# Kernel tuning notes

Measured on AMD Instinct MI355X. Metric: run time of the kernel, lower is better.

Reference implementation:

```python
import jax, jax.numpy as jnp
import numpy as np

# Static conv / spline hyperparameters (match init_kwargs)
KH = KW = 3
SH = SW = 1          # stride
DH = DW = 1          # dilation
GRID_SIZE = 5
SPLINE_ORDER = 3
N_CONVS = 8


def _extract_patches(x):
    """im2col unfold. x: (B,C,H,W) -> (B,C,Ho,Wo,KH*KW), valid padding."""
    B, C, H, W = x.shape
    Ho = (H - (KH - 1) * DH - 1) // SH + 1
    Wo = (W - (KW - 1) * DW - 1) // SW + 1
    cols = []
    for i in range(KH):
        for j in range(KW):
            cols.append(x[:, :,
                          i * DH: i * DH + (Ho - 1) * SH + 1: SH,
                          j * DW: j * DW + (Wo - 1) * SW + 1: SW])
    return jnp.stack(cols, axis=-1), Ho, Wo


def _b_splines(xf, grid):
    """Cox-de Boor recursion. xf: (P,K), grid: (K, G+2*so+1) -> (P,K,G+so)."""
    x = xf[:, :, None]
    bases = ((x >= grid[:, :-1]) & (x < grid[:, 1:])).astype(xf.dtype)
    for k in range(1, SPLINE_ORDER + 1):
        bases = ((x - grid[:, :-(k + 1)]) / (grid[:, k:-1] - grid[:, :-(k + 1)])
                 * bases[:, :, :-1]
                 + (grid[:, k + 1:] - x) / (grid[:, k + 1:] - grid[:, 1:-k])
                 * bases[:, :, 1:])
    return bases


def setup_inputs() -> dict:
    key = jax.random.key(0)
    k0, k1, k2, k3 = jax.random.split(key, 4)
    B, C, H, W = 8, 32, 64, 64
    K = KH * KW                       # in_features of KANLinear = 9
    coeff = GRID_SIZE + SPLINE_ORDER  # spline coefficients per input = 8
    # activations inside grid_range [-1, 1]
    x = jax.random.uniform(k0, (B, C, H, W), jnp.float32, -1.0, 1.0)
    # grid buffer: arange(-so, gs+so+1)*h + grid_range[0], tiled per input feature
    h = (1.0 - (-1.0)) / GRID_SIZE
    g = jnp.arange(-SPLINE_ORDER, GRID_SIZE + SPLINE_ORDER + 1,
                   dtype=jnp.float32) * h - 1.0
    grid = jnp.tile(g[None, :], (K, 1))  # (K, 12)
    base_weight = jax.random.normal(k1, (N_CONVS, K), jnp.float32) / np.sqrt(K)
    spline_weight = jax.random.normal(k2, (N_CONVS, K, coeff), jnp.float32) * 0.1
    spline_scaler = jax.random.normal(k3, (N_CONVS, K), jnp.float32) / np.sqrt(K) + 1.0
    return {"x": x, "grid": grid, "base_weight": base_weight,
            "spline_weight": spline_weight, "spline_scaler": spline_scaler}


def reference(x, grid, base_weight, spline_weight, spline_scaler):
    B, C, H, W = x.shape
    patches, Ho, Wo = _extract_patches(x)          # (B,C,Ho,Wo,K)
    K = KH * KW
    xf = patches.reshape(-1, K)                    # (P, K), P = B*C*Ho*Wo
    # KANLinear: base path (SiLU + linear) + spline path (B-spline basis + linear)
    base_out = jnp.einsum('pk,vk->pv', jax.nn.silu(xf), base_weight)
    bases = _b_splines(xf, grid)                   # (P, K, coeff)
    scaled_sw = spline_weight * spline_scaler[:, :, None]
    spline_out = jnp.einsum('pkc,vkc->pv', bases, scaled_sw)
    out = (base_out + spline_out).reshape(B, C, Ho, Wo, N_CONVS)
    # channel-major then conv ordering: out[:, kern + channel*n_convs]
    return out.transpose(0, 1, 4, 2, 3).reshape(B, C * N_CONVS, Ho, Wo)
```

## Files before the change

kernel.cpp:

```cpp
#include <hip/hip_runtime.h>

typedef _Float16 f16;
typedef _Float16 f16x8 __attribute__((ext_vector_type(8)));
typedef float    f32x4 __attribute__((ext_vector_type(4)));

#define HO 62
#define WO 62

__global__ __launch_bounds__(256, 4) void kan_conv_mfma2(
    const float* __restrict__ x,
    const float* __restrict__ grid,
    const float* __restrict__ bw,
    const float* __restrict__ sw,
    const float* __restrict__ sc,
    float* __restrict__ out)
{
    __shared__ __align__(16) f16 feat[10368];

    const int tid  = threadIdx.x;
    const int lane = tid & 63;
    const int w    = tid >> 6;

    const int bx    = blockIdx.x;
    const int plane = bx >> 3;
    const int chunk = bx & 7;
    const int r0    = chunk * 8;

    const int nn = lane & 15;
    const int kb = lane >> 4;
    f16x8 bfrag[3][2];
    #pragma unroll
    for (int ki = 0; ki < 3; ++ki) {
        #pragma unroll
        for (int kjp = 0; kjp < 2; ++kjp) {
            f16x8 bf;
            #pragma unroll
            for (int e = 0; e < 8; ++e) {
                const int k    = kb * 8 + e;
                const int kj   = kjp * 2 + (k >> 4);
                const int slot = k & 15;
                float wv = 0.0f;
                if (nn < 8 && kj < 3 && slot < 9) {
                    const int kk = ki * 3 + kj;
                    wv = (slot == 0) ? bw[nn * 9 + kk]
                                     : sw[(nn * 9 + kk) * 8 + (slot - 1)] * sc[nn * 9 + kk];
                }
                bf[e] = (f16)wv;
            }
            bfrag[ki][kjp] = bf;
        }
    }

    const float g0    = grid[0];
    const float inv_h = 1.0f / (grid[1] - grid[0]);
    const float* xp   = x + (size_t)plane * 4096;

    for (int idx = tid; idx < 640; idx += 256) {
        const int row = idx >> 6;
        const int col = idx & 63;
        int gy = r0 + row; gy = (gy < 64) ? gy : 63;
        const float xv = xp[gy * 64 + col];

        const float s = xv / (1.0f + __expf(-xv));
        const float u = (xv - g0) * inv_h;
        int j = (int)floorf(u);
        j = (j < 3) ? 3 : ((j > 7) ? 7 : j);
        const float t   = u - (float)j;
        const float omt = 1.0f - t;
        const float t2  = t * t;
        const float t3  = t2 * t;
        const float c6  = 1.0f / 6.0f;
        float bv[4];
        bv[0] = omt * omt * omt * c6;
        bv[1] = (3.0f * t3 - 6.0f * t2 + 4.0f) * c6;
        bv[2] = (-3.0f * t3 + 3.0f * t2 + 3.0f * t + 1.0f) * c6;
        bv[3] = t3 * c6;

        const int base0 = row * 1024 + col * 8;
        f16x8 z0 = {(f16)s, (f16)0.f, (f16)0.f, (f16)0.f,
                    (f16)0.f, (f16)0.f, (f16)0.f, (f16)0.f};
        f16x8 z1 = {(f16)0.f, (f16)0.f, (f16)0.f, (f16)0.f,
                    (f16)0.f, (f16)0.f, (f16)0.f, (f16)0.f};
        *(f16x8*)&feat[base0]       = z0;
        *(f16x8*)&feat[base0 + 512] = z1;
        #pragma unroll
        for (int m = 0; m < 4; ++m) {
            const int slot = j - 2 + m;
            feat[row * 1024 + (slot >> 3) * 512 + col * 8 + (slot & 7)] = (f16)bv[m];
        }
    }
    if (tid < 16) {
        f16x8 z = {(f16)0.f, (f16)0.f, (f16)0.f, (f16)0.f,
                   (f16)0.f, (f16)0.f, (f16)0.f, (f16)0.f};
        *(f16x8*)&feat[10240 + tid * 8] = z;
    }
    __syncthreads();

    const int mI    = lane & 15;
    const int khalf = kb & 1;
    const int cAdd  = kb >> 1;
    const int c0    = w * 16;
    const int aBase = khalf * 512 + (c0 + mI + cAdd) * 8;

    f16x8 af[3][2];
    #pragma unroll
    for (int kjp = 0; kjp < 2; ++kjp) {
        af[0][kjp] = *(const f16x8*)&feat[aBase + kjp * 16 + 0 * 1024];
        af[1][kjp] = *(const f16x8*)&feat[aBase + kjp * 16 + 1 * 1024];
    }

    #pragma unroll
    for (int i = 0; i < 8; ++i) {
        #pragma unroll
        for (int kjp = 0; kjp < 2; ++kjp)
            af[(i + 2) % 3][kjp] = *(const f16x8*)&feat[aBase + kjp * 16 + (i + 2) * 1024];

        f32x4 acc = {0.f, 0.f, 0.f, 0.f};
        #pragma unroll
        for (int ki = 0; ki < 3; ++ki) {
            #pragma unroll
            for (int kjp = 0; kjp < 2; ++kjp)
                acc = __builtin_amdgcn_mfma_f32_16x16x32_f16(
                          af[(i + ki) % 3][kjp], bfrag[ki][kjp], acc, 0, 0, 0);
        }

        const int ho = r0 + i;
        if (nn < 8 && ho < HO) {
            const int cb = c0 + kb * 4;
            float* po = out + ((size_t)(plane * 8 + nn) * (HO * WO)) + ho * WO + cb;
            if (cb + 3 < WO) {
                float2 lo = {acc[0], acc[1]};
                float2 hi = {acc[2], acc[3]};
                *(float2*)po       = lo;
                *(float2*)(po + 2) = hi;
            } else {
                #pragma unroll
                for (int q = 0; q < 4; ++q)
                    if (cb + q < WO) po[q] = acc[q];
            }
        }
    }
}

extern "C" void kernel_launch(void* const* d_in, const int* in_sizes, int n_in,
                              void* d_out, int out_size, void* d_ws, size_t ws_size,
                              hipStream_t stream) {
    const float* x    = (const float*)d_in[0];
    const float* grid = (const float*)d_in[1];
    const float* bw   = (const float*)d_in[2];
    const float* sw   = (const float*)d_in[3];
    const float* sc   = (const float*)d_in[4];
    float* out = (float*)d_out;

    kan_conv_mfma2<<<2048, 256, 0, stream>>>(x, grid, bw, sw, sc, out);
}
```

Measured before the change: 97.16 us.

## Give each wavefront a private feature tile to drop the block barrier

Each wavefront now computes SiLU and B-spline features for its own 10x18 halo tile into a private LDS slice. This removes the __syncthreads between feature construction and the MFMA stage, and lays features out as contiguous 16-element records per pixel. The cost is recomputing halo columns, about 180 features per wave instead of 160, and the launch bound rises to 5 blocks per CU. It relies on wavefront-level execution ordering instead of an explicit barrier for LDS visibility within the wave.

```diff
diff --git a/kernel.cpp b/kernel.cpp
--- a/kernel.cpp
+++ b/kernel.cpp
@@ -7,7 +7,7 @@
 #define HO 62
 #define WO 62
 
-__global__ __launch_bounds__(256, 4) void kan_conv_mfma2(
+__global__ __launch_bounds__(256, 5) void kan_conv_nobar(
     const float* __restrict__ x,
     const float* __restrict__ grid,
     const float* __restrict__ bw,
@@ -15,16 +15,18 @@
     const float* __restrict__ sc,
     float* __restrict__ out)
 {
-    __shared__ __align__(16) f16 feat[10368];
+    __shared__ __align__(16) f16 feat[4 * 2880];
 
     const int tid  = threadIdx.x;
     const int lane = tid & 63;
     const int w    = tid >> 6;
+    f16* wfeat = &feat[w * 2880];
 
     const int bx    = blockIdx.x;
     const int plane = bx >> 3;
     const int chunk = bx & 7;
     const int r0    = chunk * 8;
+    const int c0    = w * 16;
 
     const int nn = lane & 15;
     const int kb = lane >> 4;
@@ -51,69 +53,74 @@
         }
     }
 
+    const float* xp = x + (size_t)plane * 4096;
+    float xv3[3];
+    int   p3[3];
+    #pragma unroll
+    for (int it = 0; it < 3; ++it) {
+        int p = it * 64 + lane;
+        p3[it] = p;
+        int row = p / 18;
+        int col = p - row * 18;
+        int gy = r0 + row; gy = (gy < 64) ? gy : 63;
+        int gx = c0 + col; gx = (gx < 64) ? gx : 63;
+        xv3[it] = xp[gy * 64 + gx];
+    }
+
     const float g0    = grid[0];
     const float inv_h = 1.0f / (grid[1] - grid[0]);
-    const float* xp   = x + (size_t)plane * 4096;
 
-    for (int idx = tid; idx < 640; idx += 256) {
-        const int row = idx >> 6;
-        const int col = idx & 63;
-        int gy = r0 + row; gy = (gy < 64) ? gy : 63;
-        const float xv = xp[gy * 64 + col];
+    #pragma unroll
+    for (int it = 0; it < 3; ++it) {
+        const int p = p3[it];
+        if (p < 180) {
+            const float xv = xv3[it];
+            const float s = xv / (1.0f + __expf(-xv));
+            const float u = (xv - g0) * inv_h;
+            int j = (int)floorf(u);
+            j = (j < 3) ? 3 : ((j > 7) ? 7 : j);
+            const float t   = u - (float)j;
+            const float omt = 1.0f - t;
+            const float t2  = t * t;
+            const float t3  = t2 * t;
+            const float c6  = 1.0f / 6.0f;
+            float bv0 = omt * omt * omt * c6;
+            float bv1 = (3.0f * t3 - 6.0f * t2 + 4.0f) * c6;
+            float bv2 = (-3.0f * t3 + 3.0f * t2 + 3.0f * t + 1.0f) * c6;
+            float bv3 = t3 * c6;
 
-        const float s = xv / (1.0f + __expf(-xv));
-        const float u = (xv - g0) * inv_h;
-        int j = (int)floorf(u);
-        j = (j < 3) ? 3 : ((j > 7) ? 7 : j);
-        const float t   = u - (float)j;
-        const float omt = 1.0f - t;
-        const float t2  = t * t;
-        const float t3  = t2 * t;
-        const float c6  = 1.0f / 6.0f;
-        float bv[4];
-        bv[0] = omt * omt * omt * c6;
-        bv[1] = (3.0f * t3 - 6.0f * t2 + 4.0f) * c6;
-        bv[2] = (-3.0f * t3 + 3.0f * t2 + 3.0f * t + 1.0f) * c6;
-        bv[3] = t3 * c6;
-
-        const int base0 = row * 1024 + col * 8;
-        f16x8 z0 = {(f16)s, (f16)0.f, (f16)0.f, (f16)0.f,
-                    (f16)0.f, (f16)0.f, (f16)0.f, (f16)0.f};
-        f16x8 z1 = {(f16)0.f, (f16)0.f, (f16)0.f, (f16)0.f,
-                    (f16)0.f, (f16)0.f, (f16)0.f, (f16)0.f};
-        *(f16x8*)&feat[base0]       = z0;
-        *(f16x8*)&feat[base0 + 512] = z1;
-        #pragma unroll
-        for (int m = 0; m < 4; ++m) {
-            const int slot = j - 2 + m;
-            feat[row * 1024 + (slot >> 3) * 512 + col * 8 + (slot & 7)] = (f16)bv[m];
+            f16* fp = &wfeat[p * 16];
+            f16x8 z0 = {(f16)s, (f16)0.f, (f16)0.f, (f16)0.f,
+                        (f16)0.f, (f16)0.f, (f16)0.f, (f16)0.f};
+            f16x8 z1 = {(f16)0.f, (f16)0.f, (f16)0.f, (f16)0.f,
+                        (f16)0.f, (f16)0.f, (f16)0.f, (f16)0.f};
+            *(f16x8*)fp       = z0;
+            *(f16x8*)(fp + 8) = z1;
+            fp[j - 2] = (f16)bv0;
+            fp[j - 1] = (f16)bv1;
+            fp[j]     = (f16)bv2;
+            fp[j + 1] = (f16)bv3;
         }
     }
-    if (tid < 16) {
-        f16x8 z = {(f16)0.f, (f16)0.f, (f16)0.f, (f16)0.f,
-                   (f16)0.f, (f16)0.f, (f16)0.f, (f16)0.f};
-        *(f16x8*)&feat[10240 + tid * 8] = z;
-    }
-    __syncthreads();
 
     const int mI    = lane & 15;
     const int khalf = kb & 1;
     const int cAdd  = kb >> 1;
-    const int c0    = w * 16;
-    const int aBase = khalf * 512 + (c0 + mI + cAdd) * 8;
+    const int aBase = (mI + cAdd) * 16 + khalf * 8;
 
     f16x8 af[3][2];
     #pragma unroll
     for (int kjp = 0; kjp < 2; ++kjp) {
-        af[0][kjp] = *(const f16x8*)&feat[aBase + kjp * 16 + 0 * 1024];
-        af[1][kjp] = *(const f16x8*)&feat[aBase + kjp * 16 + 1 * 1024];
+        af[0][kjp] = *(const f16x8*)&wfeat[aBase + kjp * 32 + 0 * 288];
+        af[1][kjp] = *(const f16x8*)&wfeat[aBase + kjp * 32 + 1 * 288];
     }
 
     #pragma unroll
     for (int i = 0; i < 8; ++i) {
         #pragma unroll
         for (int kjp = 0; kjp < 2; ++kjp)
-            af[(i + 2) % 3][kjp] = *(const f16x8*)&feat[aBase + kjp * 16 + (i + 2) * 1024];
+            af[(i + 2) % 3][kjp] =
+                *(const f16x8*)&wfeat[aBase + kjp * 32 + (i + 2) * 288];
 
         f32x4 acc = {0.f, 0.f, 0.f, 0.f};
         #pragma unroll
@@ -152,5 +159,5 @@
     const float* sc   = (const float*)d_in[4];
     float* out = (float*)d_out;
 
-    kan_conv_mfma2<<<2048, 256, 0, stream>>>(x, grid, bw, sw, sc, out);
+    kan_conv_nobar<<<2048, 256, 0, stream>>>(x, grid, bw, sw, sc, out);
 }
```

New measurement: 94.27 us. 1.03x faster.
